# Kernel tuning notes

Measured on AMD Instinct MI355X. Metric: run time of the kernel, lower is better.

The kernel has to match this reference:

```python
import jax, jax.numpy as jnp
import numpy as np

N_HEADS = 4
SIGMA = 1.0


def setup_inputs() -> dict:
    key = jax.random.key(0)
    k1, k2, k3, k4, k5 = jax.random.split(key, 5)
    B, T, N, C_IN, C_OUT, K1 = 2, 12, 10000, 64, 32, 17
    x = jax.random.normal(k1, (B, T, N, C_IN), dtype=jnp.float32)
    W = jax.random.normal(k2, (C_OUT, C_IN), dtype=jnp.float32) * (1.0 / np.sqrt(C_IN))
    b = jax.random.normal(k3, (C_OUT,), dtype=jnp.float32) * 0.01
    nearest_dist = jax.random.uniform(k4, (N, K1), dtype=jnp.float32)
    nearest_nodes = jax.random.randint(k5, (N, K1), 0, N, dtype=jnp.int32)
    return {"x": x, "W": W, "b": b, "nearest_dist": nearest_dist, "nearest_nodes": nearest_nodes}


def reference(x, W, b, nearest_dist, nearest_nodes):
    # Linear projection: (B,T,N,C_in) -> (B,T,N,C_out)
    x = jnp.einsum('btni,oi->btno', x, W) + b
    B, T, N, C = x.shape
    K1 = nearest_nodes.shape[1]  # k+1
    H = N_HEADS
    # pad row of zeros at index N (also reachable via index -1, matching torch)
    pad_x = jnp.concatenate([x, jnp.zeros_like(x[:, :, :1])], axis=2)  # (B,T,N+1,C)
    lam = jnp.arange(1, H + 1, dtype=x.dtype) / H  # (H,)
    nn_flat = nearest_nodes.reshape(-1)            # (N*K1,)
    d_flat = nearest_dist.reshape(-1)              # (N*K1,)
    w = jnp.exp(-(d_flat[:, None] ** 2) * lam / (SIGMA ** 2))  # (N*K1, H)
    w = jnp.where(nn_flat[:, None] == -1, 0.0, w)
    w = jnp.where(w < 1e-5, 0.0, w)
    # gather neighbor features and reduce over neighbor axis per head
    gathered = pad_x[:, :, nn_flat].reshape(B, T, N, K1, C)  # (B,T,N,K1,C)
    wk = w.reshape(N, K1, H)
    agg = jnp.einsum('btnkc,nkh->btnhc', gathered, wk)       # (B,T,N,H,C)
    d_clean = jnp.where(jnp.isinf(d_flat), 0.0, d_flat)
    dist_agg = (w * d_clean[:, None]).reshape(N, K1, H).sum(axis=1)  # (N,H)
    return agg + dist_agg[None, None, :, :, None]
```

## Files before the change

### kernel.cpp

```cpp
#include <hip/hip_runtime.h>
#include <hip/hip_bf16.h>
#include <math.h>

#define CIN   64
#define COUT  32
#define K1V   17
#define HV    4
#define XSTR  72

typedef float v4f __attribute__((ext_vector_type(4)));
typedef unsigned int v2u __attribute__((ext_vector_type(2)));
typedef short bf8s __attribute__((ext_vector_type(8)));
typedef float f32x16 __attribute__((ext_vector_type(16)));

__device__ __forceinline__ unsigned short f2bf(float f) {
  unsigned u = __builtin_bit_cast(unsigned, f);
  unsigned r = 0x7FFFu + ((u >> 16) & 1u);
  return (unsigned short)((u + r) >> 16);
}
__device__ __forceinline__ unsigned pack2(float lo, float hi) {
  return (unsigned)f2bf(lo) | ((unsigned)f2bf(hi) << 16);
}

__global__ __launch_bounds__(256) void proj_kernel(
    const float* __restrict__ x, const float* __restrict__ W,
    const float* __restrict__ b, float* __restrict__ xp, long nrows) {
  __shared__ unsigned short Xb[128 * XSTR];
  __shared__ unsigned short Wb[32 * XSTR];
  int tid = threadIdx.x;
  long r0 = (long)blockIdx.x * 128;
  if (r0 >= nrows) return;

  {
    const v4f* wg = (const v4f*)W;
#pragma unroll
    for (int s = 0; s < 2; ++s) {
      int fi  = tid + s * 256;
      v4f wv  = wg[fi];
      int row = fi >> 4, c4 = fi & 15;
      v2u p = { pack2(wv.x, wv.y), pack2(wv.z, wv.w) };
      *(v2u*)&Wb[row * XSTR + c4 * 4] = p;
    }
  }
  {
    const v4f* xg = (const v4f*)(x + r0 * CIN);
#pragma unroll
    for (int s = 0; s < 8; ++s) {
      int fi  = tid + s * 256;
      v4f xv  = xg[fi];
      int row = fi >> 4, c4 = fi & 15;
      v2u p = { pack2(xv.x, xv.y), pack2(xv.z, xv.w) };
      *(v2u*)&Xb[row * XSTR + c4 * 4] = p;
    }
  }
  __syncthreads();

  int wv = tid >> 6;
  int l  = tid & 63;
  int lr = l & 31;
  int lh = l >> 5;

  f32x16 acc;
#pragma unroll
  for (int i = 0; i < 16; ++i) acc[i] = 0.0f;

  int arow = wv * 32 + lr;
#pragma unroll
  for (int ks = 0; ks < 4; ++ks) {
    bf8s a  = *(const bf8s*)&Xb[arow * XSTR + ks * 16 + lh * 8];
    bf8s bb = *(const bf8s*)&Wb[lr   * XSTR + ks * 16 + lh * 8];
    acc = __builtin_amdgcn_mfma_f32_32x32x16_bf16(a, bb, acc, 0, 0, 0);
  }

  float bias = b[lr];
  float* outb = xp + (r0 + wv * 32) * COUT;
#pragma unroll
  for (int r = 0; r < 16; ++r) {
    int rr = (r & 3) + 8 * (r >> 2) + 4 * lh;
    outb[(size_t)rr * COUT + lr] = acc[r] + bias;
  }
}

__global__ __launch_bounds__(256) void gcn_kernel(
    const float* __restrict__ xp,
    const float* __restrict__ dist,
    const int*   __restrict__ nn,
    float* __restrict__ out,
    int N) {
  __shared__ float wl[8][K1V][HV];
  __shared__ float dl[8][K1V];
  __shared__ int   nl[8][K1V];
  __shared__ float dagl[8][HV];

  int tid = threadIdx.x;
  int bt  = blockIdx.y;
  int n0  = blockIdx.x * 8;

  if (tid < 8 * K1V) {
    int l = tid / K1V, k = tid % K1V;
    int n_ = n0 + l;
    float w0 = 0, w1 = 0, w2 = 0, w3 = 0, dc = 0;
    int idx = 0;
    if (n_ < N) {
      float d = dist[(long)n_ * K1V + k];
      idx = nn[(long)n_ * K1V + k];
      float d2 = d * d;
      w0 = __expf(-d2 * 0.25f);
      w1 = __expf(-d2 * 0.50f);
      w2 = __expf(-d2 * 0.75f);
      w3 = __expf(-d2);
      if (idx == -1) { w0 = w1 = w2 = w3 = 0.0f; }
      if (w0 < 1e-5f) w0 = 0.0f;
      if (w1 < 1e-5f) w1 = 0.0f;
      if (w2 < 1e-5f) w2 = 0.0f;
      if (w3 < 1e-5f) w3 = 0.0f;
      dc = isinf(d) ? 0.0f : d;
      if (idx < 0 || idx >= N) idx = 0;
    }
    wl[l][k][0] = w0; wl[l][k][1] = w1; wl[l][k][2] = w2; wl[l][k][3] = w3;
    dl[l][k] = dc; nl[l][k] = idx;
  }
  __syncthreads();

  if (tid < 8 * HV) {
    int l = tid >> 2, h = tid & 3;
    float s = 0.0f;
#pragma unroll
    for (int k = 0; k < K1V; ++k) s = fmaf(wl[l][k][h], dl[l][k], s);
    dagl[l][h] = s;
  }
  __syncthreads();

  int ln = tid >> 5;
  int c  = tid & 31;
  int n  = n0 + ln;
  if (n >= N) return;

  const float* base = xp + (size_t)bt * N * COUT + c;
  float a0 = dagl[ln][0], a1 = dagl[ln][1], a2 = dagl[ln][2], a3 = dagl[ln][3];

#pragma unroll
  for (int k = 0; k < K1V; ++k) {
    int   idx = nl[ln][k];
    float v   = base[(size_t)idx * COUT];
    v4f w4 = *(const v4f*)&wl[ln][k][0];
    a0 = fmaf(w4.x, v, a0);
    a1 = fmaf(w4.y, v, a1);
    a2 = fmaf(w4.z, v, a2);
    a3 = fmaf(w4.w, v, a3);
  }

  float* ob = out + (((size_t)bt * N + n) * HV) * COUT + c;
  __builtin_nontemporal_store(a0, ob);
  __builtin_nontemporal_store(a1, ob + COUT);
  __builtin_nontemporal_store(a2, ob + 2 * COUT);
  __builtin_nontemporal_store(a3, ob + 3 * COUT);
}

extern "C" void kernel_launch(void* const* d_in, const int* in_sizes, int n_in,
                              void* d_out, int out_size, void* d_ws, size_t ws_size,
                              hipStream_t stream) {
  const float* x    = (const float*)d_in[0];
  const float* W    = (const float*)d_in[1];
  const float* b    = (const float*)d_in[2];
  const float* dist = (const float*)d_in[3];
  const int*   nn   = (const int*)d_in[4];
  float* out = (float*)d_out;
  float* xp  = (float*)d_ws;

  int  N  = in_sizes[4] / K1V;
  long M  = (long)in_sizes[0] / CIN;
  int  BT = (int)(M / N);

  proj_kernel<<<(int)((M + 127) / 128), 256, 0, stream>>>(x, W, b, xp, M);

  dim3 grid((N + 7) / 8, BT);
  gcn_kernel<<<grid, 256, 0, stream>>>(xp, dist, nn, out, N);
}
```

Before: 76.72 us.

## Store projected features in bf16 and load MFMA operands directly from global

The projection kernel now drops its shared-memory staging and loads x and W rows straight from global memory into registers, converting them to bf16 for the MFMA. The projected intermediate is written as bf16 instead of fp32, which halves the bytes written and then gathered by the GCN kernel. The cost is extra rounding of the intermediate features, and W is re-read by every wave rather than once per block.

```diff
diff --git a/kernel.cpp b/kernel.cpp
--- a/kernel.cpp
+++ b/kernel.cpp
@@ -6,83 +6,70 @@
 #define COUT  32
 #define K1V   17
 #define HV    4
-#define XSTR  72
 
 typedef float v4f __attribute__((ext_vector_type(4)));
-typedef unsigned int v2u __attribute__((ext_vector_type(2)));
+typedef unsigned int v4u __attribute__((ext_vector_type(4)));
 typedef short bf8s __attribute__((ext_vector_type(8)));
 typedef float f32x16 __attribute__((ext_vector_type(16)));
+typedef unsigned short u16;
 
-__device__ __forceinline__ unsigned short f2bf(float f) {
+__device__ __forceinline__ u16 f2bf(float f) {
   unsigned u = __builtin_bit_cast(unsigned, f);
   unsigned r = 0x7FFFu + ((u >> 16) & 1u);
-  return (unsigned short)((u + r) >> 16);
+  return (u16)((u + r) >> 16);
 }
 __device__ __forceinline__ unsigned pack2(float lo, float hi) {
   return (unsigned)f2bf(lo) | ((unsigned)f2bf(hi) << 16);
 }
+__device__ __forceinline__ float bf2f(u16 h) {
+  unsigned u = ((unsigned)h) << 16;
+  return __builtin_bit_cast(float, u);
+}
 
 __global__ __launch_bounds__(256) void proj_kernel(
     const float* __restrict__ x, const float* __restrict__ W,
-    const float* __restrict__ b, float* __restrict__ xp, long nrows) {
-  __shared__ unsigned short Xb[128 * XSTR];
-  __shared__ unsigned short Wb[32 * XSTR];
+    const float* __restrict__ b, u16* __restrict__ xp, long nrows) {
   int tid = threadIdx.x;
-  long r0 = (long)blockIdx.x * 128;
-  if (r0 >= nrows) return;
+  int wv  = tid >> 6;
+  int l   = tid & 63;
+  int lr  = l & 31;
+  int lh  = l >> 5;
+  long rbase = (long)blockIdx.x * 128 + wv * 32;
+  if (rbase + lr >= nrows) return;
 
-  {
-    const v4f* wg = (const v4f*)W;
-#pragma unroll
-    for (int s = 0; s < 2; ++s) {
-      int fi  = tid + s * 256;
-      v4f wv  = wg[fi];
-      int row = fi >> 4, c4 = fi & 15;
-      v2u p = { pack2(wv.x, wv.y), pack2(wv.z, wv.w) };
-      *(v2u*)&Wb[row * XSTR + c4 * 4] = p;
-    }
-  }
-  {
-    const v4f* xg = (const v4f*)(x + r0 * CIN);
-#pragma unroll
-    for (int s = 0; s < 8; ++s) {
-      int fi  = tid + s * 256;
-      v4f xv  = xg[fi];
-      int row = fi >> 4, c4 = fi & 15;
-      v2u p = { pack2(xv.x, xv.y), pack2(xv.z, xv.w) };
-      *(v2u*)&Xb[row * XSTR + c4 * 4] = p;
-    }
-  }
-  __syncthreads();
-
-  int wv = tid >> 6;
-  int l  = tid & 63;
-  int lr = l & 31;
-  int lh = l >> 5;
+  const float* xr = x + (rbase + lr) * CIN;
+  const float* wr = W + (long)lr * CIN;
 
   f32x16 acc;
 #pragma unroll
   for (int i = 0; i < 16; ++i) acc[i] = 0.0f;
 
-  int arow = wv * 32 + lr;
 #pragma unroll
   for (int ks = 0; ks < 4; ++ks) {
-    bf8s a  = *(const bf8s*)&Xb[arow * XSTR + ks * 16 + lh * 8];
-    bf8s bb = *(const bf8s*)&Wb[lr   * XSTR + ks * 16 + lh * 8];
-    acc = __builtin_amdgcn_mfma_f32_32x32x16_bf16(a, bb, acc, 0, 0, 0);
+    int k0 = ks * 16 + lh * 8;
+    v4f xa = *(const v4f*)(xr + k0);
+    v4f xb = *(const v4f*)(xr + k0 + 4);
+    v4f wa = *(const v4f*)(wr + k0);
+    v4f wb = *(const v4f*)(wr + k0 + 4);
+    v4u au = { pack2(xa.x, xa.y), pack2(xa.z, xa.w),
+               pack2(xb.x, xb.y), pack2(xb.z, xb.w) };
+    v4u bu = { pack2(wa.x, wa.y), pack2(wa.z, wa.w),
+               pack2(wb.x, wb.y), pack2(wb.z, wb.w) };
+    acc = __builtin_amdgcn_mfma_f32_32x32x16_bf16(
+        __builtin_bit_cast(bf8s, au), __builtin_bit_cast(bf8s, bu), acc, 0, 0, 0);
   }
 
   float bias = b[lr];
-  float* outb = xp + (r0 + wv * 32) * COUT;
+  u16* outb = xp + rbase * COUT;
 #pragma unroll
   for (int r = 0; r < 16; ++r) {
     int rr = (r & 3) + 8 * (r >> 2) + 4 * lh;
-    outb[(size_t)rr * COUT + lr] = acc[r] + bias;
+    outb[(size_t)rr * COUT + lr] = f2bf(acc[r] + bias);
   }
 }
 
 __global__ __launch_bounds__(256) void gcn_kernel(
-    const float* __restrict__ xp,
+    const u16*   __restrict__ xp,
     const float* __restrict__ dist,
     const int*   __restrict__ nn,
     float* __restrict__ out,
@@ -136,13 +123,13 @@
   int n  = n0 + ln;
   if (n >= N) return;
 
-  const float* base = xp + (size_t)bt * N * COUT + c;
+  const u16* base = xp + (size_t)bt * N * COUT + c;
   float a0 = dagl[ln][0], a1 = dagl[ln][1], a2 = dagl[ln][2], a3 = dagl[ln][3];
 
 #pragma unroll
   for (int k = 0; k < K1V; ++k) {
     int   idx = nl[ln][k];
-    float v   = base[(size_t)idx * COUT];
+    float v   = bf2f(base[(size_t)idx * COUT]);
     v4f w4 = *(const v4f*)&wl[ln][k][0];
     a0 = fmaf(w4.x, v, a0);
     a1 = fmaf(w4.y, v, a1);
@@ -166,7 +153,7 @@
   const float* dist = (const float*)d_in[3];
   const int*   nn   = (const int*)d_in[4];
   float* out = (float*)d_out;
-  float* xp  = (float*)d_ws;
+  u16*   xp  = (u16*)d_ws;
 
   int  N  = in_sizes[4] / K1V;
   long M  = (long)in_sizes[0] / CIN;
```

Measured after the change: 70.04 us. 1.1x faster.
